# Optimization experiments

Measured on AMD Instinct MI355X. Metric: run time of the kernel, lower is better.

## Reference

```python
import jax, jax.numpy as jnp
import numpy as np

N_LAYERS = 4
N_WIRES = 10


def _apply_1q(state, U, wire, n):
    # state: [B, 2^n] complex64; U: [2,2] or [B,2,2]
    B = state.shape[0]
    a, b = 2 ** wire, 2 ** (n - wire - 1)
    s = state.reshape(B, a, 2, b)
    if U.ndim == 2:
        s = jnp.einsum('ij,bxjy->bxiy', U, s)
    else:
        s = jnp.einsum('bij,bxjy->bxiy', U, s)
    return s.reshape(B, -1)


def _apply_cnot(state, c, t, n):
    # CNOT with control c, target t (wire 0 = most significant bit, PennyLane convention)
    B = state.shape[0]
    q1, q2 = min(c, t), max(c, t)
    d1, d2, d3 = 2 ** q1, 2 ** (q2 - q1 - 1), 2 ** (n - q2 - 1)
    s = state.reshape(B, d1, 2, d2, 2, d3)
    if c < t:
        # control on axis 2, flip (X) target axis 4 where control bit == 1
        s = jnp.concatenate([s[:, :, 0:1], jnp.flip(s[:, :, 1:2], axis=4)], axis=2)
    else:
        # control on axis 4, flip target axis 2 where control bit == 1
        s = jnp.concatenate([s[:, :, :, :, 0:1], jnp.flip(s[:, :, :, :, 1:2], axis=2)], axis=4)
    return s.reshape(B, -1)


def _ry_mat(theta):
    # theta: [B] -> [B,2,2] complex64
    c, s = jnp.cos(theta / 2), jnp.sin(theta / 2)
    return jnp.stack([jnp.stack([c, -s], -1), jnp.stack([s, c], -1)], -2).astype(jnp.complex64)


def _rot_mat(phi, theta, omega):
    # qml.Rot(phi, theta, omega) = RZ(omega) @ RY(theta) @ RZ(phi)
    e = lambda a: jnp.exp(1j * a.astype(jnp.complex64))
    c = jnp.cos(theta / 2).astype(jnp.complex64)
    s = jnp.sin(theta / 2).astype(jnp.complex64)
    m00 = e(-0.5 * (phi + omega)) * c
    m01 = -e(0.5 * (phi - omega)) * s
    m10 = e(-0.5 * (phi - omega)) * s
    m11 = e(0.5 * (phi + omega)) * c
    return jnp.stack([jnp.stack([m00, m01]), jnp.stack([m10, m11])])


def setup_inputs() -> dict:
    key = jax.random.key(0)
    kx, kw = jax.random.split(key)
    X = jax.random.uniform(kx, (16384, N_WIRES), dtype=jnp.float32)
    # weightsStrongly = pi * U(0,1) of shape (n_layers, n_wires, 3)
    weights = np.pi * jax.random.uniform(kw, (N_LAYERS, N_WIRES, 3), dtype=jnp.float32)
    bias = jnp.zeros((1,), dtype=jnp.float32)
    return {"X": X, "weights": weights, "bias": bias}


def reference(X, weights, bias):
    B, n = X.shape
    L = weights.shape[0]
    # |0...0> batched statevector
    state = jnp.zeros((B, 2 ** n), dtype=jnp.complex64).at[:, 0].set(1.0)
    # angle encoding, gates='Y': RY(x_i * pi/2) on wire i (per-sample angle)
    for w in range(n):
        state = _apply_1q(state, _ry_mat(X[:, w] * (np.pi / 2)), w, n)
    # StronglyEntanglingLayers: Rot on each wire, then ring of CNOTs with range r_l
    for l in range(L):
        for w in range(n):
            U = _rot_mat(weights[l, w, 0], weights[l, w, 1], weights[l, w, 2])
            state = _apply_1q(state, U, w, n)
        r = l % (n - 1) + 1
        for w in range(n):
            state = _apply_cnot(state, w, (w + r) % n, n)
    # numClasses=2 -> single measurement: expval(PauliZ(wire n-1)) (last wire = LSB)
    probs = (state.real ** 2 + state.imag ** 2).reshape(B, 2 ** (n - 1), 2)
    z = jnp.sum(probs[..., 0] - probs[..., 1], axis=-1)  # [B]
    return z[:, None] + bias[None, :]  # [B, 1]
```

## Files before the change

kernel.cpp:

```cpp
#include <hip/hip_runtime.h>
#include <cstdint>
#include <utility>

#define NW 10
#define NL 4


typedef float v2 __attribute__((ext_vector_type(2)));

struct Cols10 { unsigned c[10]; };
struct Rows10 { unsigned r[10]; };

constexpr Cols10 TMAT = {{
    0x001, 0x002, 0x004, 0x008,
    0x070, 0x080, 0x100, 0x130, 0x210, 0x200
}};

constexpr unsigned tmap(unsigned m) {
    unsigned r = 0;
    for (int b = 0; b < 10; ++b) if ((m >> b) & 1u) r ^= TMAT.c[b];
    return r;
}

constexpr Rows10 invertT() {
    unsigned a[10] = {}, inv[10] = {};
    for (int i = 0; i < 10; ++i) {
        for (int j = 0; j < 10; ++j) a[i] |= ((TMAT.c[j] >> i) & 1u) << j;
        inv[i] = 1u << i;
    }
    for (int col = 0; col < 10; ++col) {
        int piv = -1;
        for (int r2 = col; r2 < 10; ++r2) if ((a[r2] >> col) & 1u) { piv = r2; break; }
        unsigned ta = a[piv]; a[piv] = a[col]; a[col] = ta;
        unsigned ti = inv[piv]; inv[piv] = inv[col]; inv[col] = ti;
        for (int r2 = 0; r2 < 10; ++r2)
            if (r2 != col && ((a[r2] >> col) & 1u)) { a[r2] ^= a[col]; inv[r2] ^= inv[col]; }
    }
    Rows10 R{};
    for (int i = 0; i < 10; ++i) R.r[i] = inv[i];
    return R;
}
constexpr Rows10 RROW = invertT();

constexpr unsigned rmap(unsigned rowmask) {
    unsigned r = 0;
    for (int b = 0; b < 10; ++b) if ((rowmask >> b) & 1u) r ^= RROW.r[b];
    return r;
}

static_assert(RROW.r[0] == 1 && RROW.r[1] == 2 && RROW.r[2] == 4 && RROW.r[3] == 8, "slot rows");
static_assert((RROW.r[4] & 15) == 0 && (RROW.r[5] & 15) == 0 && (RROW.r[6] & 15) == 0 &&
              (RROW.r[7] & 15) == 0 && (RROW.r[8] & 15) == 0 && (RROW.r[9] & 15) == 0, "lane rows");

struct Plan {
    int n;
    uint16_t pmask[40];
    uint16_t rmask[40];
    uint8_t  lw[40];
    uint16_t measmask;
};

constexpr bool keep_rot(int l, int w) {
    if (l <= 1) return true;
    if (l == 2) return w != 7;
    return w == 1 || w == 5 || w == 9;
}

constexpr int engine_class(unsigned pm) {
    const unsigned lm = pm >> 4;
    if (lm == 0) return 0;
    if (lm == 1 || lm == 2 || lm == 3 || lm == 7 || lm == 15) return 1;
    return 2;
}

constexpr Plan make_plan() {
    Plan P{};
    unsigned row[10], cI[10];
    for (int b = 0; b < 10; ++b) { row[b] = 1u << b; cI[b] = 1u << b; }
    P.n = 0;
    for (int l = 0; l < NL; ++l) {
        unsigned pm[10] = {}, rm[10] = {};
        int lw[10] = {}, cls[10] = {}, cnt = 0;
        for (int w = 0; w < NW; ++w) {
            if (l > 0 && keep_rot(l, w)) {
                const int b = 9 - w;
                pm[cnt] = tmap(cI[b]);
                rm[cnt] = rmap(row[b]);
                lw[cnt] = l * NW + w;
                cls[cnt] = engine_class(pm[cnt]);
                cnt++;
            }
        }
        int dsIdx[10] = {}, otIdx[10] = {};
        int nds = 0, not_ = 0;
        for (int i = 0; i < cnt; ++i) {
            if (cls[i] == 2) dsIdx[nds++] = i; else otIdx[not_++] = i;
        }
        int di = 0, oi = 0;
        while (di < nds || oi < not_) {
            if (di < nds) {
                const int i = dsIdx[di++];
                P.pmask[P.n] = (uint16_t)pm[i];
                P.rmask[P.n] = (uint16_t)rm[i];
                P.lw[P.n]    = (uint8_t)lw[i];
                P.n++;
            }
            if (oi < not_) {
                const int i = otIdx[oi++];
                P.pmask[P.n] = (uint16_t)pm[i];
                P.rmask[P.n] = (uint16_t)rm[i];
                P.lw[P.n]    = (uint8_t)lw[i];
                P.n++;
            }
        }
        const int r = l % (NW - 1) + 1;
        for (int w = 0; w < NW; ++w) {
            const int cb = 9 - w, tb = 9 - ((w + r) % NW);
            row[tb] ^= row[cb];
            cI[cb]  ^= cI[tb];
        }
    }
    P.measmask = (uint16_t)rmap(row[0]);
    return P;
}

constexpr Plan PL = make_plan();
constexpr int NROT = 22;
static_assert(PL.n == NROT, "plan size mismatch");

constexpr int LSEL[6] = {
    (int)(RROW.r[9] >> 4), (int)(RROW.r[8] >> 4), (int)(RROW.r[7] >> 4),
    (int)(RROW.r[6] >> 4), (int)(RROW.r[5] >> 4), (int)(RROW.r[4] >> 4)
};

template<int MASK>
__device__ __forceinline__ float swz(float v, int lane) {
    if constexpr (MASK == 1) {
        return __int_as_float(__builtin_amdgcn_mov_dpp(__float_as_int(v), 0xB1, 0xF, 0xF, true));
    } else if constexpr (MASK == 2) {
        return __int_as_float(__builtin_amdgcn_mov_dpp(__float_as_int(v), 0x4E, 0xF, 0xF, true));
    } else if constexpr (MASK == 3) {
        return __int_as_float(__builtin_amdgcn_mov_dpp(__float_as_int(v), 0x1B, 0xF, 0xF, true));
    } else if constexpr (MASK == 7) {
        return __int_as_float(__builtin_amdgcn_mov_dpp(__float_as_int(v), 0x141, 0xF, 0xF, true));
    } else if constexpr (MASK == 15) {
        return __int_as_float(__builtin_amdgcn_mov_dpp(__float_as_int(v), 0x140, 0xF, 0xF, true));
    } else if constexpr (MASK < 32) {
        return __int_as_float(__builtin_amdgcn_ds_swizzle(
            __float_as_int(v), (MASK << 10) | 0x1F));
    } else {
        return __int_as_float(__builtin_amdgcn_ds_bpermute(
            (lane << 2) ^ (MASK << 2), __float_as_int(v)));
    }
}

template<int MASK>
__device__ __forceinline__ v2 swz2(v2 v, int lane) {
    v2 r;
    r.x = swz<MASK>(v.x, lane);
    r.y = swz<MASK>(v.y, lane);
    return r;
}

__device__ __forceinline__ v2 mkv2(float a, float b) { v2 r; r.x = a; r.y = b; return r; }

__device__ __forceinline__ void cmul2(v2 ar, v2 ai, v2 br, v2 bi, v2& cr, v2& ci) {
    cr = ar * br - ai * bi;
    ci = ar * bi + ai * br;
}

__device__ __forceinline__ void upd(v2& xr, v2& xi, v2 pr, v2 pi,
                                    float cmr, float coi, float bmi, float bor,
                                    bool S) {
    const float emi = S ? -bmi : bmi;
    const float eor = S ? -bor : bor;
    const v2 nr = cmr * xr - emi * xi + eor * pr - coi * pi;
    const v2 ni = cmr * xi + emi * xr + eor * pi + coi * pr;
    xr = nr; xi = ni;
}

template<int G>
__device__ __forceinline__ void apply_rot(v2 (&sr)[16], v2 (&si)[16],
                                          const float4* __restrict__ ws,
                                          int lane) {
    constexpr unsigned pm = PL.pmask[G], rm = PL.rmask[G];
    constexpr int pLoc = pm & 15, pLane = (int)(pm >> 4);
    constexpr int rLoc = rm & 15, rLane = (int)(rm >> 4);
    const float4 m = ws[PL.lw[G]];
    const bool rl = (__popc(lane & rLane) & 1) != 0;
    const float cmr = m.x, coi = m.w;
    const float bmi = rl ? -m.y : m.y;
    const float bor = rl ? -m.z : m.z;

    if constexpr (pLane == 0) {
#pragma unroll
        for (int j = 0; j < 16; ++j) {
            const int k = j ^ pLoc;
            if (j < k) {
                const v2 ajr = sr[j], aji = si[j];
                const v2 akr = sr[k], aki = si[k];
                upd(sr[j], si[j], akr, aki, cmr, coi, bmi, bor,
                    (__builtin_popcount(j & rLoc) & 1) != 0);
                upd(sr[k], si[k], ajr, aji, cmr, coi, bmi, bor,
                    (__builtin_popcount(k & rLoc) & 1) != 0);
            }
        }
    } else if constexpr (pLoc == 0) {
#pragma unroll
        for (int j = 0; j < 16; ++j) {
            const v2 pr = swz2<pLane>(sr[j], lane);
            const v2 pi = swz2<pLane>(si[j], lane);
            upd(sr[j], si[j], pr, pi, cmr, coi, bmi, bor,
                (__builtin_popcount(j & rLoc) & 1) != 0);
        }
    } else {
#pragma unroll
        for (int j = 0; j < 16; ++j) {
            const int k = j ^ pLoc;
            if (j < k) {
                const v2 pjr = swz2<pLane>(sr[k], lane);
                const v2 pji = swz2<pLane>(si[k], lane);
                const v2 pkr = swz2<pLane>(sr[j], lane);
                const v2 pki = swz2<pLane>(si[j], lane);
                upd(sr[j], si[j], pjr, pji, cmr, coi, bmi, bor,
                    (__builtin_popcount(j & rLoc) & 1) != 0);
                upd(sr[k], si[k], pkr, pki, cmr, coi, bmi, bor,
                    (__builtin_popcount(k & rLoc) & 1) != 0);
            }
        }
    }
}

template<int... Gs>
__device__ __forceinline__ void apply_all(v2 (&sr)[16], v2 (&si)[16],
                                          const float4* __restrict__ ws,
                                          int lane,
                                          std::integer_sequence<int, Gs...>) {
    (apply_rot<Gs>(sr, si, ws, lane), ...);
}

__global__ void prep_kernel(const float* __restrict__ W, float4* __restrict__ ws) {
    const int t = threadIdx.x;
    if (t < NL * NW) {
        const float phi = W[t * 3 + 0], th = W[t * 3 + 1], om = W[t * 3 + 2];
        float sh, ch; sincosf(0.5f * th, &sh, &ch);
        float s0, c0; sincosf(-0.5f * (phi + om), &s0, &c0);
        float s1, c1; sincosf( 0.5f * (phi - om), &s1, &c1);
        ws[t] = make_float4(c0 * ch, s0 * ch, -c1 * sh, -s1 * sh);
    }
}

__global__ __launch_bounds__(256, 2) void vqc_kernel(const float* __restrict__ X,
                                                     const float4* __restrict__ ws,
                                                     const float* __restrict__ bias,
                                                     float* __restrict__ out,
                                                     int n_pairs) {
    const int t = threadIdx.x;
    const int wave = (blockIdx.x * blockDim.x + t) >> 6;
    const int lane = t & 63;
    if (wave >= n_pairs) return;

    const float* xp = X + (size_t)(2 * wave) * NW;

    v2 hr, hi;
#pragma unroll
    for (int w = 0; w < 6; ++w) {
        float s0, c0, s1, c1;
        __sincosf(xp[w]      * 0.78539816339744831f, &s0, &c0);
        __sincosf(xp[w + NW] * 0.78539816339744831f, &s1, &c1);
        const v2 s = mkv2(s0, s1), c = mkv2(c0, c1);
        const float4 m = ws[w];
        const v2 a0r = m.x * c + m.z * s;
        const v2 a0i = m.y * c + m.w * s;
        const v2 a1r = m.x * s - m.z * c;
        const v2 a1i = m.w * c - m.y * s;
        const bool b = (__popc(lane & LSEL[w]) & 1) != 0;
        const v2 br = b ? a1r : a0r;
        const v2 bi = b ? a1i : a0i;
        if (w == 0) { hr = br; hi = bi; }
        else {
            v2 nr, ni; cmul2(hr, hi, br, bi, nr, ni);
            hr = nr; hi = ni;
        }
    }
    v2 t0r[4], t0i[4], t1r[4], t1i[4];
#pragma unroll
    for (int w = 6; w < 10; ++w) {
        float s0, c0, s1, c1;
        __sincosf(xp[w]      * 0.78539816339744831f, &s0, &c0);
        __sincosf(xp[w + NW] * 0.78539816339744831f, &s1, &c1);
        const v2 s = mkv2(s0, s1), c = mkv2(c0, c1);
        const float4 m = ws[w];
        t0r[w - 6] = m.x * c + m.z * s;
        t0i[w - 6] = m.y * c + m.w * s;
        t1r[w - 6] = m.x * s - m.z * c;
        t1i[w - 6] = m.w * c - m.y * s;
    }
    v2 Ar[4], Ai[4], Br[4], Bi[4];
#pragma unroll
    for (int u = 0; u < 4; ++u) {
        const int hb = (u >> 1) & 1, lb = u & 1;
        cmul2(hb ? t1r[0] : t0r[0], hb ? t1i[0] : t0i[0],
              lb ? t1r[1] : t0r[1], lb ? t1i[1] : t0i[1], Ar[u], Ai[u]);
        cmul2(hb ? t1r[2] : t0r[2], hb ? t1i[2] : t0i[2],
              lb ? t1r[3] : t0r[3], lb ? t1i[3] : t0i[3], Br[u], Bi[u]);
    }
    v2 HAr[4], HAi[4];
#pragma unroll
    for (int u = 0; u < 4; ++u) cmul2(hr, hi, Ar[u], Ai[u], HAr[u], HAi[u]);

    v2 sr[16], si[16];
#pragma unroll
    for (int j = 0; j < 16; ++j) {
        cmul2(HAr[j >> 2], HAi[j >> 2], Br[j & 3], Bi[j & 3], sr[j], si[j]);
    }

    apply_all(sr, si, ws, lane, std::make_integer_sequence<int, NROT>{});

    constexpr unsigned mm = PL.measmask;
    constexpr int mLoc = mm & 15, mLane = (int)(mm >> 4);
    v2 acc = mkv2(0.0f, 0.0f);
#pragma unroll
    for (int j = 0; j < 16; ++j) {
        const v2 p = sr[j] * sr[j] + si[j] * si[j];
        if (__builtin_popcount(j & mLoc) & 1) acc -= p; else acc += p;
    }
    if (__popc(lane & mLane) & 1) acc = -acc;
    acc += swz2<1>(acc, lane);
    acc += swz2<2>(acc, lane);
    acc += swz2<4>(acc, lane);
    acc += swz2<8>(acc, lane);
    acc += swz2<16>(acc, lane);
    acc += swz2<32>(acc, lane);
    if (lane == 0) {
        const float b0 = bias[0];
        out[2 * wave]     = acc.x + b0;
        out[2 * wave + 1] = acc.y + b0;
    }
}

extern "C" void kernel_launch(void* const* d_in, const int* in_sizes, int n_in,
                              void* d_out, int out_size, void* d_ws, size_t ws_size,
                              hipStream_t stream) {
    const float* X    = (const float*)d_in[0];
    const float* W    = (const float*)d_in[1];
    const float* bias = (const float*)d_in[2];
    float* out = (float*)d_out;
    float4* ws = (float4*)d_ws;
    const int n_samples = in_sizes[0] / NW;
    const int n_pairs = n_samples / 2;
    const int threads = 256;
    const int blocks = (n_pairs * 64 + threads - 1) / threads;
    hipLaunchKernelGGL(prep_kernel, dim3(1), dim3(64), 0, stream, W, ws);
    hipLaunchKernelGGL(vqc_kernel, dim3(blocks), dim3(threads), 0, stream,
                       X, (const float4*)ws, bias, out, n_pairs);
}
```

Before: 125.5 us.

## Fuse rotation-coefficient prep into main kernel via per-lane compute and readlane broadcast

Removes the separate prep kernel launch. Each wave now computes one gate's rotation coefficients per lane and broadcasts them to the whole wave with readlane, instead of loading float4s from a workspace buffer. Input X loads go through a wave-uniform pointer so they can become scalar loads, and the last butterfly step of the reduction is replaced by readlane adds. In exchange every wave repeats the 40 sincos coefficient computations and adds several readlane instructions.

```diff
diff --git a/kernel.cpp b/kernel.cpp
--- a/kernel.cpp
+++ b/kernel.cpp
@@ -164,6 +164,10 @@
 
 __device__ __forceinline__ v2 mkv2(float a, float b) { v2 r; r.x = a; r.y = b; return r; }
 
+__device__ __forceinline__ float rdl(float v, int srclane) {
+    return __int_as_float(__builtin_amdgcn_readlane(__float_as_int(v), srclane));
+}
+
 __device__ __forceinline__ void cmul2(v2 ar, v2 ai, v2 br, v2 bi, v2& cr, v2& ci) {
     cr = ar * br - ai * bi;
     ci = ar * bi + ai * br;
@@ -181,16 +185,19 @@
 
 template<int G>
 __device__ __forceinline__ void apply_rot(v2 (&sr)[16], v2 (&si)[16],
-                                          const float4* __restrict__ ws,
+                                          float cfx, float cfy, float cfz, float cfw,
                                           int lane) {
     constexpr unsigned pm = PL.pmask[G], rm = PL.rmask[G];
     constexpr int pLoc = pm & 15, pLane = (int)(pm >> 4);
     constexpr int rLoc = rm & 15, rLane = (int)(rm >> 4);
-    const float4 m = ws[PL.lw[G]];
+    constexpr int gl = PL.lw[G];
+    const float cmr = rdl(cfx, gl);
+    const float myy = rdl(cfy, gl);
+    const float mzz = rdl(cfz, gl);
+    const float coi = rdl(cfw, gl);
     const bool rl = (__popc(lane & rLane) & 1) != 0;
-    const float cmr = m.x, coi = m.w;
-    const float bmi = rl ? -m.y : m.y;
-    const float bor = rl ? -m.z : m.z;
+    const float bmi = rl ? -myy : myy;
+    const float bor = rl ? -mzz : mzz;
 
     if constexpr (pLane == 0) {
 #pragma unroll
@@ -233,25 +240,14 @@
 
 template<int... Gs>
 __device__ __forceinline__ void apply_all(v2 (&sr)[16], v2 (&si)[16],
-                                          const float4* __restrict__ ws,
+                                          float cfx, float cfy, float cfz, float cfw,
                                           int lane,
                                           std::integer_sequence<int, Gs...>) {
-    (apply_rot<Gs>(sr, si, ws, lane), ...);
-}
-
-__global__ void prep_kernel(const float* __restrict__ W, float4* __restrict__ ws) {
-    const int t = threadIdx.x;
-    if (t < NL * NW) {
-        const float phi = W[t * 3 + 0], th = W[t * 3 + 1], om = W[t * 3 + 2];
-        float sh, ch; sincosf(0.5f * th, &sh, &ch);
-        float s0, c0; sincosf(-0.5f * (phi + om), &s0, &c0);
-        float s1, c1; sincosf( 0.5f * (phi - om), &s1, &c1);
-        ws[t] = make_float4(c0 * ch, s0 * ch, -c1 * sh, -s1 * sh);
-    }
+    (apply_rot<Gs>(sr, si, cfx, cfy, cfz, cfw, lane), ...);
 }
 
 __global__ __launch_bounds__(256, 2) void vqc_kernel(const float* __restrict__ X,
-                                                     const float4* __restrict__ ws,
+                                                     const float* __restrict__ W,
                                                      const float* __restrict__ bias,
                                                      float* __restrict__ out,
                                                      int n_pairs) {
@@ -260,20 +256,37 @@
     const int lane = t & 63;
     if (wave >= n_pairs) return;
 
-    const float* xp = X + (size_t)(2 * wave) * NW;
+    float cfx, cfy, cfz, cfw;
+    {
+        const int g = (lane < NL * NW) ? lane : 0;
+        const float phi = W[g * 3 + 0], th = W[g * 3 + 1], om = W[g * 3 + 2];
+        float sh, ch; __sincosf(0.5f * th, &sh, &ch);
+        float s0, c0; __sincosf(-0.5f * (phi + om), &s0, &c0);
+        float s1, c1; __sincosf( 0.5f * (phi - om), &s1, &c1);
+        cfx = c0 * ch; cfy = s0 * ch; cfz = -c1 * sh; cfw = -s1 * sh;
+    }
+
+    const uintptr_t pbits = (uintptr_t)(X + (size_t)(2 * wave) * NW);
+    const float* xp = (const float*)(
+        ((uintptr_t)(uint32_t)__builtin_amdgcn_readfirstlane((uint32_t)(pbits >> 32)) << 32) |
+        (uintptr_t)(uint32_t)__builtin_amdgcn_readfirstlane((uint32_t)pbits));
+    float xv[2 * NW];
+#pragma unroll
+    for (int i = 0; i < 2 * NW; ++i) xv[i] = xp[i];
 
     v2 hr, hi;
 #pragma unroll
     for (int w = 0; w < 6; ++w) {
         float s0, c0, s1, c1;
-        __sincosf(xp[w]      * 0.78539816339744831f, &s0, &c0);
-        __sincosf(xp[w + NW] * 0.78539816339744831f, &s1, &c1);
+        __sincosf(xv[w]      * 0.78539816339744831f, &s0, &c0);
+        __sincosf(xv[w + NW] * 0.78539816339744831f, &s1, &c1);
         const v2 s = mkv2(s0, s1), c = mkv2(c0, c1);
-        const float4 m = ws[w];
-        const v2 a0r = m.x * c + m.z * s;
-        const v2 a0i = m.y * c + m.w * s;
-        const v2 a1r = m.x * s - m.z * c;
-        const v2 a1i = m.w * c - m.y * s;
+        const float mx = rdl(cfx, w), my = rdl(cfy, w);
+        const float mz = rdl(cfz, w), mw = rdl(cfw, w);
+        const v2 a0r = mx * c + mz * s;
+        const v2 a0i = my * c + mw * s;
+        const v2 a1r = mx * s - mz * c;
+        const v2 a1i = mw * c - my * s;
         const bool b = (__popc(lane & LSEL[w]) & 1) != 0;
         const v2 br = b ? a1r : a0r;
         const v2 bi = b ? a1i : a0i;
@@ -287,14 +300,15 @@
 #pragma unroll
     for (int w = 6; w < 10; ++w) {
         float s0, c0, s1, c1;
-        __sincosf(xp[w]      * 0.78539816339744831f, &s0, &c0);
-        __sincosf(xp[w + NW] * 0.78539816339744831f, &s1, &c1);
+        __sincosf(xv[w]      * 0.78539816339744831f, &s0, &c0);
+        __sincosf(xv[w + NW] * 0.78539816339744831f, &s1, &c1);
         const v2 s = mkv2(s0, s1), c = mkv2(c0, c1);
-        const float4 m = ws[w];
-        t0r[w - 6] = m.x * c + m.z * s;
-        t0i[w - 6] = m.y * c + m.w * s;
-        t1r[w - 6] = m.x * s - m.z * c;
-        t1i[w - 6] = m.w * c - m.y * s;
+        const float mx = rdl(cfx, w), my = rdl(cfy, w);
+        const float mz = rdl(cfz, w), mw = rdl(cfw, w);
+        t0r[w - 6] = mx * c + mz * s;
+        t0i[w - 6] = my * c + mw * s;
+        t1r[w - 6] = mx * s - mz * c;
+        t1i[w - 6] = mw * c - my * s;
     }
     v2 Ar[4], Ai[4], Br[4], Bi[4];
 #pragma unroll
@@ -315,7 +329,8 @@
         cmul2(HAr[j >> 2], HAi[j >> 2], Br[j & 3], Bi[j & 3], sr[j], si[j]);
     }
 
-    apply_all(sr, si, ws, lane, std::make_integer_sequence<int, NROT>{});
+    apply_all(sr, si, cfx, cfy, cfz, cfw, lane,
+              std::make_integer_sequence<int, NROT>{});
 
     constexpr unsigned mm = PL.measmask;
     constexpr int mLoc = mm & 15, mLane = (int)(mm >> 4);
@@ -331,11 +346,12 @@
     acc += swz2<4>(acc, lane);
     acc += swz2<8>(acc, lane);
     acc += swz2<16>(acc, lane);
-    acc += swz2<32>(acc, lane);
+    const float sx = rdl(acc.x, 0) + rdl(acc.x, 32);
+    const float sy = rdl(acc.y, 0) + rdl(acc.y, 32);
     if (lane == 0) {
         const float b0 = bias[0];
-        out[2 * wave]     = acc.x + b0;
-        out[2 * wave + 1] = acc.y + b0;
+        out[2 * wave]     = sx + b0;
+        out[2 * wave + 1] = sy + b0;
     }
 }
 
@@ -346,12 +362,10 @@
     const float* W    = (const float*)d_in[1];
     const float* bias = (const float*)d_in[2];
     float* out = (float*)d_out;
-    float4* ws = (float4*)d_ws;
     const int n_samples = in_sizes[0] / NW;
     const int n_pairs = n_samples / 2;
     const int threads = 256;
     const int blocks = (n_pairs * 64 + threads - 1) / threads;
-    hipLaunchKernelGGL(prep_kernel, dim3(1), dim3(64), 0, stream, W, ws);
     hipLaunchKernelGGL(vqc_kernel, dim3(blocks), dim3(threads), 0, stream,
-                       X, (const float4*)ws, bias, out, n_pairs);
-}
+                       X, W, bias, out, n_pairs);
+}
```

After: 123.0 us. 1.02x faster.
